# Performance work log

Hardware: AMD Instinct MI355X
Metric: run time of the kernel (lower is better)

Reference implementation:

```python
import jax, jax.numpy as jnp
import numpy as np

E, D, H, N = 8, 1024, 4096, 8192  # experts, model dim, moe intermediate, total tokens


def setup_inputs() -> dict:
    key = jax.random.key(0)
    k0, k1, k2, k3 = jax.random.split(key, 4)
    x = jax.random.normal(k0, (N, D), jnp.float32)
    # PrimeRL layout: w1,w3: [E, H, D]; w2: [E, D, H]
    w1 = jax.random.normal(k1, (E, H, D), jnp.float32) * 0.02
    w2 = jax.random.normal(k2, (E, D, H), jnp.float32) * 0.02
    w3 = jax.random.normal(k3, (E, H, D), jnp.float32) * 0.02
    num_tokens_per_expert = jnp.full((E,), N // E, dtype=jnp.int32)  # balanced, sums to N
    return {"x": x, "w1": w1, "w2": w2, "w3": w3,
            "num_tokens_per_expert": num_tokens_per_expert}


def reference(x, w1, w2, w3, num_tokens_per_expert):
    # grouped MoE FFN: per expert e over its contiguous token block,
    #   h = gelu_tanh(x @ w1[e].T) * (x @ w3[e].T); out = h @ w2[e].T
    # torch path casts to bf16 for the grouped mm, casts output back.
    gs = num_tokens_per_expert.astype(jnp.int32)  # group sizes = offsets via cumsum
    xb = x.astype(jnp.bfloat16)
    w1t = jnp.swapaxes(w1, -2, -1).astype(jnp.bfloat16)  # [E, D, H]
    w2t = jnp.swapaxes(w2, -2, -1).astype(jnp.bfloat16)  # [E, H, D]
    w3t = jnp.swapaxes(w3, -2, -1).astype(jnp.bfloat16)  # [E, D, H]
    g = jax.lax.ragged_dot(xb, w1t, gs)                  # [N, H]
    h = jax.nn.gelu(g, approximate=True) * jax.lax.ragged_dot(xb, w3t, gs)
    out = jax.lax.ragged_dot(h, w2t, gs).astype(x.dtype)  # [N, D]
    return out
```

## Files before the change

### kernel.cpp

```cpp
#include <hip/hip_runtime.h>
#include <hip/hip_bf16.h>

#define E_ 8
#define D_ 1024
#define H_ 4096
#define N_ 8192

typedef __attribute__((ext_vector_type(8))) short bf16x8;
typedef __attribute__((ext_vector_type(4))) float f32x4;
typedef __attribute__((ext_vector_type(4))) float fv4;
typedef unsigned short u16;

static __device__ __forceinline__ u16 f2bf(float f) {
    unsigned int u = __float_as_uint(f);
    u += 0x7fffu + ((u >> 16) & 1u);
    return (u16)(u >> 16);
}

static __device__ __forceinline__ void st_bf4(u16* p, float4 v) {
    union { u16 u[4]; unsigned long long ll; } t;
    t.u[0] = f2bf(v.x); t.u[1] = f2bf(v.y); t.u[2] = f2bf(v.z); t.u[3] = f2bf(v.w);
    *(unsigned long long*)p = t.ll;
}

static __device__ __forceinline__ float gelu_tanh(float x) {
    float x3 = x * x * x;
    float z = 0.7978845608028654f * (x + 0.044715f * x3);
    float t = 1.0f - 2.0f / (1.0f + __expf(2.0f * z));
    return 0.5f * x * (1.0f + t);
}

static __device__ __forceinline__ int expert_of(const int* __restrict__ ntpe, int row) {
    int acc = 0;
    #pragma unroll
    for (int i = 0; i < E_; ++i) {
        acc += ntpe[i];
        if (row < acc) return i;
    }
    return E_ - 1;
}

#define GLD16(gp, lp) __builtin_amdgcn_global_load_lds( \
    (const __attribute__((address_space(1))) void*)(gp), \
    (__attribute__((address_space(3))) void*)(lp), 16, 0, 0)

#define CVT_XBLK 512
#define CVT_WBLK 2048
#define CVT_NBLK (CVT_XBLK + 3 * CVT_WBLK)

__global__ __launch_bounds__(256) void cvt_all2(
    const float* __restrict__ x, const float* __restrict__ w1,
    const float* __restrict__ w2, const float* __restrict__ w3,
    u16* __restrict__ xb, u16* __restrict__ w1b,
    u16* __restrict__ w2b, u16* __restrict__ w3b)
{
    int b = blockIdx.x;
    const float* src; u16* dst; int n8; int b0; int nb; bool nts = false;
    if (b < CVT_WBLK) {
        src = w2; dst = w2b; n8 = E_ * D_ * H_ / 8; b0 = 0; nb = CVT_WBLK; nts = true;
    } else if (b < 2 * CVT_WBLK) {
        src = w1; dst = w1b; n8 = E_ * H_ * D_ / 8; b0 = CVT_WBLK; nb = CVT_WBLK;
    } else if (b < 3 * CVT_WBLK) {
        src = w3; dst = w3b; n8 = E_ * H_ * D_ / 8; b0 = 2 * CVT_WBLK; nb = CVT_WBLK;
    } else {
        src = x; dst = xb; n8 = N_ * D_ / 8; b0 = 3 * CVT_WBLK; nb = CVT_XBLK;
    }
    int t = (b - b0) * 256 + threadIdx.x;
    int stride = nb * 256;
    const fv4* s4 = (const fv4*)src;
    for (int i = t; i < n8; i += stride) {
        fv4 a = __builtin_nontemporal_load(s4 + (size_t)i * 2);
        fv4 c = __builtin_nontemporal_load(s4 + (size_t)i * 2 + 1);
        union { u16 u[8]; bf16x8 v; } o;
        o.u[0] = f2bf(a.x); o.u[1] = f2bf(a.y); o.u[2] = f2bf(a.z); o.u[3] = f2bf(a.w);
        o.u[4] = f2bf(c.x); o.u[5] = f2bf(c.y); o.u[6] = f2bf(c.z); o.u[7] = f2bf(c.w);
        if (nts) __builtin_nontemporal_store(o.v, (bf16x8*)(dst + (size_t)i * 8));
        else *(bf16x8*)(dst + (size_t)i * 8) = o.v;
    }
}


#define EPIT 72

__global__ __launch_bounds__(256, 3) void moe_gemm13_fast(
    const u16* __restrict__ xb, const u16* __restrict__ w1b,
    const u16* __restrict__ w3b, const int* __restrict__ ntpe,
    u16* __restrict__ hbuf)
{
    __shared__ u16 smem[16384];
    u16* sA  = smem;
    u16* sB1 = smem + 8192;
    u16* sB2 = smem + 12288;

    const int tid = threadIdx.x;
    const int bswz = (blockIdx.x & 7) * (4096 / 8) + (blockIdx.x >> 3);
    const int eg = bswz >> 9;
    const int rr = bswz & 511;
    const int m0 = (eg * 8 + (rr & 7)) * 128;
    const int n0 = (rr >> 3) * 64;
    const int e = expert_of(ntpe, m0);
    const int wave = tid >> 6, lane = tid & 63;
    const int wm = (wave >> 1) * 64, wn = (wave & 1) * 32;
    const int fr = lane & 15, quad = lane >> 4;
    const int sw = fr & 7;

    const u16* Ag  = xb  + (size_t)m0 * D_;
    const u16* B1g = w1b + ((size_t)e * H_ + n0) * D_;
    const u16* B2g = w3b + ((size_t)e * H_ + n0) * D_;

    const int srr = lane >> 3;
    const int scg = ((lane & 7) ^ srr) * 8;

    f32x4 accg[4][2], accu[4][2];
    #pragma unroll
    for (int i = 0; i < 4; ++i)
        #pragma unroll
        for (int j = 0; j < 2; ++j) {
            accg[i][j] = (f32x4){0.f, 0.f, 0.f, 0.f};
            accu[i][j] = (f32x4){0.f, 0.f, 0.f, 0.f};
        }

    for (int k0 = 0; k0 < D_; k0 += 64) {
        #pragma unroll
        for (int c = 0; c < 4; ++c)
            GLD16(Ag + (size_t)(wave * 32 + c * 8 + srr) * D_ + k0 + scg,
                  sA + (wave * 32 + c * 8) * 64);
        #pragma unroll
        for (int c = 0; c < 2; ++c) {
            GLD16(B1g + (size_t)(wave * 16 + c * 8 + srr) * D_ + k0 + scg,
                  sB1 + (wave * 16 + c * 8) * 64);
            GLD16(B2g + (size_t)(wave * 16 + c * 8 + srr) * D_ + k0 + scg,
                  sB2 + (wave * 16 + c * 8) * 64);
        }
        __syncthreads();

        #pragma unroll
        for (int kh = 0; kh < 2; ++kh) {
            const int ks = ((quad + kh * 4) ^ sw) * 8;
            bf16x8 fa[4], fb1[2], fb2[2];
            #pragma unroll
            for (int i = 0; i < 4; ++i)
                fa[i] = *(const bf16x8*)(&sA[(wm + i * 16 + fr) * 64 + ks]);
            #pragma unroll
            for (int j = 0; j < 2; ++j) {
                fb1[j] = *(const bf16x8*)(&sB1[(wn + j * 16 + fr) * 64 + ks]);
                fb2[j] = *(const bf16x8*)(&sB2[(wn + j * 16 + fr) * 64 + ks]);
            }
            #pragma unroll
            for (int i = 0; i < 4; ++i)
                #pragma unroll
                for (int j = 0; j < 2; ++j) {
                    accg[i][j] = __builtin_amdgcn_mfma_f32_16x16x32_bf16(fa[i], fb1[j], accg[i][j], 0, 0, 0);
                    accu[i][j] = __builtin_amdgcn_mfma_f32_16x16x32_bf16(fa[i], fb2[j], accu[i][j], 0, 0, 0);
                }
        }
        __syncthreads();
    }

    #pragma unroll
    for (int i = 0; i < 4; ++i) {
        int rl = wm + i * 16 + quad * 4;
        #pragma unroll
        for (int j = 0; j < 2; ++j) {
            int cl = wn + j * 16 + fr;
            #pragma unroll
            for (int r = 0; r < 4; ++r) {
                float hv = gelu_tanh(accg[i][j][r]) * accu[i][j][r];
                smem[(rl + r) * EPIT + cl] = f2bf(hv);
            }
        }
    }
    __syncthreads();
    #pragma unroll
    for (int it = 0; it < 4; ++it) {
        int chunk = it * 256 + tid;
        int row = chunk >> 3;
        int col = (chunk & 7) * 8;
        bf16x8 v = *(const bf16x8*)(&smem[row * EPIT + col]);
        *(bf16x8*)(&hbuf[(size_t)(m0 + row) * H_ + n0 + col]) = v;
    }
}

__global__ __launch_bounds__(256, 3) void moe_gemm2_fast(
    const u16* __restrict__ hbuf, const u16* __restrict__ w2b,
    const int* __restrict__ ntpe, float* __restrict__ out)
{
    __shared__ u16 smem[16384];
    u16* sA = smem;
    u16* sB = smem + 8192;

    const int tid = threadIdx.x;
    const int bswz = (blockIdx.x & 7) * (512 / 8) + (blockIdx.x >> 3);
    const int eg = bswz >> 6;
    const int rr = bswz & 63;
    const int m0 = (eg * 8 + (rr & 7)) * 128;
    const int n0 = (rr >> 3) * 128;
    const int e = expert_of(ntpe, m0);
    const int wave = tid >> 6, lane = tid & 63;
    const int wm = (wave >> 1) * 64, wn = (wave & 1) * 64;
    const int fr = lane & 15, quad = lane >> 4;
    const int sw = fr & 7;

    const u16* Ag = hbuf + (size_t)m0 * H_;
    const u16* Bg = w2b + ((size_t)e * D_ + n0) * H_;

    const int srr = lane >> 3;
    const int scg = ((lane & 7) ^ srr) * 8;

    f32x4 acc[4][4];
    #pragma unroll
    for (int i = 0; i < 4; ++i)
        #pragma unroll
        for (int j = 0; j < 4; ++j)
            acc[i][j] = (f32x4){0.f, 0.f, 0.f, 0.f};

    for (int k0 = 0; k0 < H_; k0 += 64) {
        #pragma unroll
        for (int c = 0; c < 4; ++c) {
            GLD16(Ag + (size_t)(wave * 32 + c * 8 + srr) * H_ + k0 + scg,
                  sA + (wave * 32 + c * 8) * 64);
            GLD16(Bg + (size_t)(wave * 32 + c * 8 + srr) * H_ + k0 + scg,
                  sB + (wave * 32 + c * 8) * 64);
        }
        __syncthreads();

        #pragma unroll
        for (int kh = 0; kh < 2; ++kh) {
            const int ks = ((quad + kh * 4) ^ sw) * 8;
            bf16x8 fa[4], fb[4];
            #pragma unroll
            for (int i = 0; i < 4; ++i) {
                fa[i] = *(const bf16x8*)(&sA[(wm + i * 16 + fr) * 64 + ks]);
                fb[i] = *(const bf16x8*)(&sB[(wn + i * 16 + fr) * 64 + ks]);
            }
            #pragma unroll
            for (int i = 0; i < 4; ++i)
                #pragma unroll
                for (int j = 0; j < 4; ++j)
                    acc[i][j] = __builtin_amdgcn_mfma_f32_16x16x32_bf16(fa[i], fb[j], acc[i][j], 0, 0, 0);
        }
        __syncthreads();
    }

    #pragma unroll
    for (int i = 0; i < 4; ++i) {
        int rowb = m0 + wm + i * 16 + quad * 4;
        #pragma unroll
        for (int j = 0; j < 4; ++j) {
            int col = n0 + wn + j * 16 + fr;
            #pragma unroll
            for (int r = 0; r < 4; ++r)
                __builtin_nontemporal_store(acc[i][j][r], &out[(size_t)(rowb + r) * D_ + col]);
        }
    }
}

#define LDSP 40

__global__ __launch_bounds__(256, 2) void moe_gemm13_slow(
    const float* __restrict__ x, const float* __restrict__ w1,
    const float* __restrict__ w3, const int* __restrict__ ntpe,
    u16* __restrict__ hbuf)
{
    const int tid = threadIdx.x;
    const int m0 = blockIdx.y * 128, n0 = blockIdx.x * 128;
    const int e = expert_of(ntpe, m0);
    __shared__ u16 sA[128][LDSP]; __shared__ u16 sB1[128][LDSP]; __shared__ u16 sB2[128][LDSP];
    const int wave = tid >> 6, lane = tid & 63;
    const int wm = (wave >> 1) * 64, wn = (wave & 1) * 64;
    const int fr = lane & 15, quad = lane >> 4;
    f32x4 accg[4][4], accu[4][4];
    #pragma unroll
    for (int i = 0; i < 4; ++i)
        #pragma unroll
        for (int j = 0; j < 4; ++j) {
            accg[i][j] = (f32x4){0.f,0.f,0.f,0.f}; accu[i][j] = (f32x4){0.f,0.f,0.f,0.f};
        }
    const float* Ab  = x  + (size_t)m0 * D_;
    const float* B1b = w1 + ((size_t)e * H_ + n0) * D_;
    const float* B2b = w3 + ((size_t)e * H_ + n0) * D_;
    for (int k0 = 0; k0 < D_; k0 += 32) {
        #pragma unroll
        for (int s = 0; s < 4; ++s) {
            int idx = s * 256 + tid;
            int row = idx >> 3, col = (idx & 7) * 4;
            size_t go = (size_t)row * D_ + k0 + col;
            st_bf4(&sA[row][col],  *(const float4*)(Ab + go));
            st_bf4(&sB1[row][col], *(const float4*)(B1b + go));
            st_bf4(&sB2[row][col], *(const float4*)(B2b + go));
        }
        __syncthreads();
        bf16x8 fa[4], fb1[4], fb2[4];
        #pragma unroll
        for (int i = 0; i < 4; ++i) {
            fa[i]  = *(const bf16x8*)(&sA[wm + i * 16 + fr][quad * 8]);
            fb1[i] = *(const bf16x8*)(&sB1[wn + i * 16 + fr][quad * 8]);
            fb2[i] = *(const bf16x8*)(&sB2[wn + i * 16 + fr][quad * 8]);
        }
        #pragma unroll
        for (int i = 0; i < 4; ++i)
            #pragma unroll
            for (int j = 0; j < 4; ++j) {
                accg[i][j] = __builtin_amdgcn_mfma_f32_16x16x32_bf16(fa[i], fb1[j], accg[i][j], 0, 0, 0);
                accu[i][j] = __builtin_amdgcn_mfma_f32_16x16x32_bf16(fa[i], fb2[j], accu[i][j], 0, 0, 0);
            }
        __syncthreads();
    }
    #pragma unroll
    for (int i = 0; i < 4; ++i) {
        int rowb = m0 + wm + i * 16 + quad * 4;
        #pragma unroll
        for (int j = 0; j < 4; ++j) {
            int col = n0 + wn + j * 16 + fr;
            #pragma unroll
            for (int r = 0; r < 4; ++r)
                hbuf[(size_t)(rowb + r) * H_ + col] = f2bf(gelu_tanh(accg[i][j][r]) * accu[i][j][r]);
        }
    }
}

__global__ __launch_bounds__(256, 2) void moe_gemm2_slow(
    const u16* __restrict__ hbuf, const float* __restrict__ w2,
    const int* __restrict__ ntpe, float* __restrict__ out)
{
    const int tid = threadIdx.x;
    const int m0 = blockIdx.y * 128, n0 = blockIdx.x * 128;
    const int e = expert_of(ntpe, m0);
    __shared__ u16 sA[128][LDSP]; __shared__ u16 sB[128][LDSP];
    const int wave = tid >> 6, lane = tid & 63;
    const int wm = (wave >> 1) * 64, wn = (wave & 1) * 64;
    const int fr = lane & 15, quad = lane >> 4;
    f32x4 acc[4][4];
    #pragma unroll
    for (int i = 0; i < 4; ++i)
        #pragma unroll
        for (int j = 0; j < 4; ++j) acc[i][j] = (f32x4){0.f,0.f,0.f,0.f};
    const u16* Ab = hbuf + (size_t)m0 * H_;
    const float* Bb = w2 + ((size_t)e * D_ + n0) * H_;
    for (int k0 = 0; k0 < H_; k0 += 32) {
        #pragma unroll
        for (int s = 0; s < 2; ++s) {
            int idx = s * 256 + tid;
            int row = idx >> 2, col = (idx & 3) * 8;
            *(bf16x8*)(&sA[row][col]) = *(const bf16x8*)(Ab + (size_t)row * H_ + k0 + col);
        }
        #pragma unroll
        for (int s = 0; s < 4; ++s) {
            int idx = s * 256 + tid;
            int row = idx >> 3, col = (idx & 7) * 4;
            st_bf4(&sB[row][col], *(const float4*)(Bb + (size_t)row * H_ + k0 + col));
        }
        __syncthreads();
        bf16x8 fa[4], fb[4];
        #pragma unroll
        for (int i = 0; i < 4; ++i) {
            fa[i] = *(const bf16x8*)(&sA[wm + i * 16 + fr][quad * 8]);
            fb[i] = *(const bf16x8*)(&sB[wn + i * 16 + fr][quad * 8]);
        }
        #pragma unroll
        for (int i = 0; i < 4; ++i)
            #pragma unroll
            for (int j = 0; j < 4; ++j)
                acc[i][j] = __builtin_amdgcn_mfma_f32_16x16x32_bf16(fa[i], fb[j], acc[i][j], 0, 0, 0);
        __syncthreads();
    }
    #pragma unroll
    for (int i = 0; i < 4; ++i) {
        int rowb = m0 + wm + i * 16 + quad * 4;
        #pragma unroll
        for (int j = 0; j < 4; ++j) {
            int col = n0 + wn + j * 16 + fr;
            #pragma unroll
            for (int r = 0; r < 4; ++r)
                out[(size_t)(rowb + r) * D_ + col] = acc[i][j][r];
        }
    }
}

extern "C" void kernel_launch(void* const* d_in, const int* in_sizes, int n_in,
                              void* d_out, int out_size, void* d_ws, size_t ws_size,
                              hipStream_t stream) {
    const float* x  = (const float*)d_in[0];
    const float* w1 = (const float*)d_in[1];
    const float* w2 = (const float*)d_in[2];
    const float* w3 = (const float*)d_in[3];
    const int* ntpe = (const int*)d_in[4];
    float* out = (float*)d_out;

    const size_t SZ_XB = (size_t)N_ * D_ * 2;
    const size_t SZ_W  = (size_t)E_ * H_ * D_ * 2;
    const size_t SZ_H  = (size_t)N_ * H_ * 2;
    const size_t NEED  = SZ_XB + 3 * SZ_W + SZ_H;

    if (ws_size >= NEED) {
        char* p = (char*)d_ws;
        u16* xb  = (u16*)p;                 p += SZ_XB;
        u16* w1b = (u16*)p;                 p += SZ_W;
        u16* w3b = (u16*)p;                 p += SZ_W;
        u16* w2b = (u16*)p;                 p += SZ_W;
        u16* hb  = (u16*)p;

        cvt_all2<<<CVT_NBLK, 256, 0, stream>>>(x, w1, w2, w3, xb, w1b, w2b, w3b);

        moe_gemm13_fast<<<4096, 256, 0, stream>>>(xb, w1b, w3b, ntpe, hb);

        moe_gemm2_fast<<<512, 256, 0, stream>>>(hb, w2b, ntpe, out);
    } else {
        u16* hb = (u16*)d_ws;
        dim3 g1(H_ / 128, N_ / 128);
        moe_gemm13_slow<<<g1, 256, 0, stream>>>(x, w1, w3, ntpe, hb);
        dim3 g2(D_ / 128, N_ / 128);
        moe_gemm2_slow<<<g2, 256, 0, stream>>>(hb, w2, ntpe, out);
    }
}
```

Measured before the change: 618.7 us.

## Double-buffer LDS tiles in both MoE GEMM kernels to overlap loads with MFMA

Both GEMM kernels now use two shared-memory buffers. The next K-tile's global-to-LDS loads are issued before the MFMA work on the current tile, which is meant to hide global memory latency behind compute. The main loop is restructured to step 128 along K per iteration, with one barrier per 64-wide half-step instead of two. In exchange, LDS use per block doubles to 64 KB and launch bounds drop from 3 to 2 blocks per CU, lowering occupancy.

Measured after the change: 625.2 us. No clear change (+1.0%).

```diff
diff --git a/kernel.cpp b/kernel.cpp
--- a/kernel.cpp
+++ b/kernel.cpp
@@ -82,15 +82,50 @@
 
 #define EPIT 72
 
-__global__ __launch_bounds__(256, 3) void moe_gemm13_fast(
+#define G13_STAGE(SB, KK) do { \
+    _Pragma("unroll") \
+    for (int c_ = 0; c_ < 4; ++c_) \
+        GLD16(Ag + (size_t)(wave * 32 + c_ * 8 + srr) * D_ + (KK) + scg, \
+              (SB) + (wave * 32 + c_ * 8) * 64); \
+    _Pragma("unroll") \
+    for (int c_ = 0; c_ < 2; ++c_) { \
+        GLD16(B1g + (size_t)(wave * 16 + c_ * 8 + srr) * D_ + (KK) + scg, \
+              (SB) + 8192 + (wave * 16 + c_ * 8) * 64); \
+        GLD16(B2g + (size_t)(wave * 16 + c_ * 8 + srr) * D_ + (KK) + scg, \
+              (SB) + 12288 + (wave * 16 + c_ * 8) * 64); \
+    } \
+} while (0)
+
+#define G13_COMPUTE(SB) do { \
+    _Pragma("unroll") \
+    for (int kh_ = 0; kh_ < 2; ++kh_) { \
+        const int ks_ = ((quad + kh_ * 4) ^ sw) * 8; \
+        bf16x8 fa_[4], fb1_[2], fb2_[2]; \
+        _Pragma("unroll") \
+        for (int i_ = 0; i_ < 4; ++i_) \
+            fa_[i_] = *(const bf16x8*)(&(SB)[(wm + i_ * 16 + fr) * 64 + ks_]); \
+        _Pragma("unroll") \
+        for (int j_ = 0; j_ < 2; ++j_) { \
+            fb1_[j_] = *(const bf16x8*)(&(SB)[8192 + (wn + j_ * 16 + fr) * 64 + ks_]); \
+            fb2_[j_] = *(const bf16x8*)(&(SB)[12288 + (wn + j_ * 16 + fr) * 64 + ks_]); \
+        } \
+        _Pragma("unroll") \
+        for (int i_ = 0; i_ < 4; ++i_) \
+            _Pragma("unroll") \
+            for (int j_ = 0; j_ < 2; ++j_) { \
+                accg[i_][j_] = __builtin_amdgcn_mfma_f32_16x16x32_bf16(fa_[i_], fb1_[j_], accg[i_][j_], 0, 0, 0); \
+                accu[i_][j_] = __builtin_amdgcn_mfma_f32_16x16x32_bf16(fa_[i_], fb2_[j_], accu[i_][j_], 0, 0, 0); \
+            } \
+    } \
+} while (0)
+
+__global__ __launch_bounds__(256, 2) void moe_gemm13_fast(
     const u16* __restrict__ xb, const u16* __restrict__ w1b,
     const u16* __restrict__ w3b, const int* __restrict__ ntpe,
     u16* __restrict__ hbuf)
 {
-    __shared__ u16 smem[16384];
-    u16* sA  = smem;
-    u16* sB1 = smem + 8192;
-    u16* sB2 = smem + 12288;
+    __shared__ u16 smem0[16384];
+    __shared__ u16 smem1[16384];
 
     const int tid = threadIdx.x;
     const int bswz = (blockIdx.x & 7) * (4096 / 8) + (blockIdx.x >> 3);
@@ -120,40 +155,16 @@
             accu[i][j] = (f32x4){0.f, 0.f, 0.f, 0.f};
         }
 
-    for (int k0 = 0; k0 < D_; k0 += 64) {
-        #pragma unroll
-        for (int c = 0; c < 4; ++c)
-            GLD16(Ag + (size_t)(wave * 32 + c * 8 + srr) * D_ + k0 + scg,
-                  sA + (wave * 32 + c * 8) * 64);
-        #pragma unroll
-        for (int c = 0; c < 2; ++c) {
-            GLD16(B1g + (size_t)(wave * 16 + c * 8 + srr) * D_ + k0 + scg,
-                  sB1 + (wave * 16 + c * 8) * 64);
-            GLD16(B2g + (size_t)(wave * 16 + c * 8 + srr) * D_ + k0 + scg,
-                  sB2 + (wave * 16 + c * 8) * 64);
-        }
-        __syncthreads();
-
-        #pragma unroll
-        for (int kh = 0; kh < 2; ++kh) {
-            const int ks = ((quad + kh * 4) ^ sw) * 8;
-            bf16x8 fa[4], fb1[2], fb2[2];
-            #pragma unroll
-            for (int i = 0; i < 4; ++i)
-                fa[i] = *(const bf16x8*)(&sA[(wm + i * 16 + fr) * 64 + ks]);
-            #pragma unroll
-            for (int j = 0; j < 2; ++j) {
-                fb1[j] = *(const bf16x8*)(&sB1[(wn + j * 16 + fr) * 64 + ks]);
-                fb2[j] = *(const bf16x8*)(&sB2[(wn + j * 16 + fr) * 64 + ks]);
-            }
-            #pragma unroll
-            for (int i = 0; i < 4; ++i)
-                #pragma unroll
-                for (int j = 0; j < 2; ++j) {
-                    accg[i][j] = __builtin_amdgcn_mfma_f32_16x16x32_bf16(fa[i], fb1[j], accg[i][j], 0, 0, 0);
-                    accu[i][j] = __builtin_amdgcn_mfma_f32_16x16x32_bf16(fa[i], fb2[j], accu[i][j], 0, 0, 0);
-                }
-        }
+    G13_STAGE(smem0, 0);
+    __syncthreads();
+
+    #pragma unroll 2
+    for (int k0 = 0; k0 < D_; k0 += 128) {
+        G13_STAGE(smem1, k0 + 64);
+        G13_COMPUTE(smem0);
+        __syncthreads();
+        if (k0 + 128 < D_) G13_STAGE(smem0, k0 + 128);
+        G13_COMPUTE(smem1);
         __syncthreads();
     }
 
@@ -166,7 +177,7 @@
             #pragma unroll
             for (int r = 0; r < 4; ++r) {
                 float hv = gelu_tanh(accg[i][j][r]) * accu[i][j][r];
-                smem[(rl + r) * EPIT + cl] = f2bf(hv);
+                smem0[(rl + r) * EPIT + cl] = f2bf(hv);
             }
         }
     }
@@ -176,18 +187,45 @@
         int chunk = it * 256 + tid;
         int row = chunk >> 3;
         int col = (chunk & 7) * 8;
-        bf16x8 v = *(const bf16x8*)(&smem[row * EPIT + col]);
+        bf16x8 v = *(const bf16x8*)(&smem0[row * EPIT + col]);
         *(bf16x8*)(&hbuf[(size_t)(m0 + row) * H_ + n0 + col]) = v;
     }
 }
 
-__global__ __launch_bounds__(256, 3) void moe_gemm2_fast(
+#define G2_STAGE(SB, KK) do { \
+    _Pragma("unroll") \
+    for (int c_ = 0; c_ < 4; ++c_) { \
+        GLD16(Ag + (size_t)(wave * 32 + c_ * 8 + srr) * H_ + (KK) + scg, \
+              (SB) + (wave * 32 + c_ * 8) * 64); \
+        GLD16(Bg + (size_t)(wave * 32 + c_ * 8 + srr) * H_ + (KK) + scg, \
+              (SB) + 8192 + (wave * 32 + c_ * 8) * 64); \
+    } \
+} while (0)
+
+#define G2_COMPUTE(SB) do { \
+    _Pragma("unroll") \
+    for (int kh_ = 0; kh_ < 2; ++kh_) { \
+        const int ks_ = ((quad + kh_ * 4) ^ sw) * 8; \
+        bf16x8 fa_[4], fb_[4]; \
+        _Pragma("unroll") \
+        for (int i_ = 0; i_ < 4; ++i_) { \
+            fa_[i_] = *(const bf16x8*)(&(SB)[(wm + i_ * 16 + fr) * 64 + ks_]); \
+            fb_[i_] = *(const bf16x8*)(&(SB)[8192 + (wn + i_ * 16 + fr) * 64 + ks_]); \
+        } \
+        _Pragma("unroll") \
+        for (int i_ = 0; i_ < 4; ++i_) \
+            _Pragma("unroll") \
+            for (int j_ = 0; j_ < 4; ++j_) \
+                acc[i_][j_] = __builtin_amdgcn_mfma_f32_16x16x32_bf16(fa_[i_], fb_[j_], acc[i_][j_], 0, 0, 0); \
+    } \
+} while (0)
+
+__global__ __launch_bounds__(256, 2) void moe_gemm2_fast(
     const u16* __restrict__ hbuf, const u16* __restrict__ w2b,
     const int* __restrict__ ntpe, float* __restrict__ out)
 {
-    __shared__ u16 smem[16384];
-    u16* sA = smem;
-    u16* sB = smem + 8192;
+    __shared__ u16 smem0[16384];
+    __shared__ u16 smem1[16384];
 
     const int tid = threadIdx.x;
     const int bswz = (blockIdx.x & 7) * (512 / 8) + (blockIdx.x >> 3);
@@ -214,31 +252,15 @@
         for (int j = 0; j < 4; ++j)
             acc[i][j] = (f32x4){0.f, 0.f, 0.f, 0.f};
 
-    for (int k0 = 0; k0 < H_; k0 += 64) {
-        #pragma unroll
-        for (int c = 0; c < 4; ++c) {
-            GLD16(Ag + (size_t)(wave * 32 + c * 8 + srr) * H_ + k0 + scg,
-                  sA + (wave * 32 + c * 8) * 64);
-            GLD16(Bg + (size_t)(wave * 32 + c * 8 + srr) * H_ + k0 + scg,
-                  sB + (wave * 32 + c * 8) * 64);
-        }
-        __syncthreads();
-
-        #pragma unroll
-        for (int kh = 0; kh < 2; ++kh) {
-            const int ks = ((quad + kh * 4) ^ sw) * 8;
-            bf16x8 fa[4], fb[4];
-            #pragma unroll
-            for (int i = 0; i < 4; ++i) {
-                fa[i] = *(const bf16x8*)(&sA[(wm + i * 16 + fr) * 64 + ks]);
-                fb[i] = *(const bf16x8*)(&sB[(wn + i * 16 + fr) * 64 + ks]);
-            }
-            #pragma unroll
-            for (int i = 0; i < 4; ++i)
-                #pragma unroll
-                for (int j = 0; j < 4; ++j)
-                    acc[i][j] = __builtin_amdgcn_mfma_f32_16x16x32_bf16(fa[i], fb[j], acc[i][j], 0, 0, 0);
-        }
+    G2_STAGE(smem0, 0);
+    __syncthreads();
+
+    for (int k0 = 0; k0 < H_; k0 += 128) {
+        G2_STAGE(smem1, k0 + 64);
+        G2_COMPUTE(smem0);
+        __syncthreads();
+        if (k0 + 128 < H_) G2_STAGE(smem0, k0 + 128);
+        G2_COMPUTE(smem1);
         __syncthreads();
     }
 
```
